# Optimization experiments

Hardware: AMD Instinct MI355X
Metric: run time of the kernel (lower is better)

Reference implementation:

```python
import jax, jax.numpy as jnp
import numpy as np

ENT_TOTAL = 500000
REL_TOTAL = 1000
H = 128
B = 1024
K = 10  # negative_ent + negative_rel
MARGIN = 1.0


def setup_inputs() -> dict:
    key = jax.random.key(0)
    ks = jax.random.split(key, 8)
    return {
        "ent_embeddings": jax.random.normal(ks[0], (ENT_TOTAL, H), dtype=jnp.float32) * 0.05,
        "rel_matrices": jax.random.normal(ks[1], (REL_TOTAL, H * H), dtype=jnp.float32) * 0.05,
        "pos_h": jax.random.randint(ks[2], (B,), 0, ENT_TOTAL, dtype=jnp.int32),
        "pos_t": jax.random.randint(ks[3], (B,), 0, ENT_TOTAL, dtype=jnp.int32),
        "pos_r": jax.random.randint(ks[4], (B,), 0, REL_TOTAL, dtype=jnp.int32),
        "neg_h": jax.random.randint(ks[5], (B * K,), 0, ENT_TOTAL, dtype=jnp.int32),
        "neg_t": jax.random.randint(ks[6], (B * K,), 0, ENT_TOTAL, dtype=jnp.int32),
        "neg_r": jax.random.randint(ks[7], (B * K,), 0, REL_TOTAL, dtype=jnp.int32),
    }


def _calc_score(ent_emb, rel_mat, h_idx, t_idx, r_idx):
    # gather embeddings / relation matrices per example
    h = ent_emb[h_idx]                          # [N, H]
    t = ent_emb[t_idx]                          # [N, H]
    r = rel_mat[r_idx].reshape(-1, H, H)        # [N, H, H]
    # h * (r @ t), then sum over hidden dim -> per-example score [N]
    rt = jnp.einsum('nij,nj->ni', r, t)         # [N, H]
    return jnp.sum(h * rt, axis=-1)             # [N]


def reference(ent_embeddings, rel_matrices, pos_h, pos_t, pos_r, neg_h, neg_t, neg_r):
    p_score = _calc_score(ent_embeddings, rel_matrices, pos_h, pos_t, pos_r)  # [B]
    n_all = _calc_score(ent_embeddings, rel_matrices, neg_h, neg_t, neg_r)    # [B*K]
    # mean over the K negatives per positive (matches reduce_mean over axis 1)
    n_score = jnp.mean(n_all.reshape(B, K), axis=1)                           # [B]
    loss = jnp.sum(jnp.maximum(n_score - p_score + MARGIN, 0.0))
    return loss
```

## Files before the change

kernel.cpp:

```cpp
#include <hip/hip_runtime.h>

#define H 128
#define BPOS 1024
#define KNEG 10
#define NPOS 1024
#define NNEG (BPOS * KNEG)
#define NTOT (NPOS + NNEG)

__global__ __launch_bounds__(256) void rescal_score_kernel(
    const float* __restrict__ ent,
    const float* __restrict__ rel,
    const int* __restrict__ pos_h, const int* __restrict__ pos_t,
    const int* __restrict__ pos_r,
    const int* __restrict__ neg_h, const int* __restrict__ neg_t,
    const int* __restrict__ neg_r,
    float* __restrict__ scores)
{
    const int n   = blockIdx.x;
    const int tid = threadIdx.x;

    int h_idx, t_idx, r_idx;
    if (n < NPOS) {
        h_idx = pos_h[n]; t_idx = pos_t[n]; r_idx = pos_r[n];
    } else {
        const int m = n - NPOS;
        h_idx = neg_h[m]; t_idx = neg_t[m]; r_idx = neg_r[m];
    }

    __shared__ float sh[H];
    __shared__ float st[H];
    if (tid < H) {
        sh[tid] = ent[(size_t)h_idx * H + tid];
    } else {
        st[tid - H] = ent[(size_t)t_idx * H + (tid - H)];
    }
    __syncthreads();

    const float4* __restrict__ R4 =
        (const float4*)(rel + (size_t)r_idx * (H * H));

    const int jbase = (4 * tid) & 127;
    const float4 t4 = *(const float4*)&st[jbase];

    float acc = 0.0f;
    const int ibase = tid >> 5;
#pragma unroll
    for (int k = 0; k < 16; ++k) {
        const float4 r4 = R4[k * 256 + tid];
        const float  hi = sh[8 * k + ibase];
        acc += hi * (r4.x * t4.x + r4.y * t4.y + r4.z * t4.z + r4.w * t4.w);
    }

#pragma unroll
    for (int off = 32; off > 0; off >>= 1)
        acc += __shfl_down(acc, off, 64);

    __shared__ float red[4];
    const int wave = tid >> 6;
    if ((tid & 63) == 0) red[wave] = acc;
    __syncthreads();
    if (tid == 0)
        scores[n] = red[0] + red[1] + red[2] + red[3];
}

__global__ __launch_bounds__(1024) void rescal_loss_kernel(
    const float* __restrict__ scores,
    float* __restrict__ out)
{
    const int b = threadIdx.x;
    const float p = scores[b];
    const float* __restrict__ neg = scores + NPOS + b * KNEG;
    float ns = 0.0f;
#pragma unroll
    for (int k = 0; k < KNEG; ++k) ns += neg[k];
    ns *= (1.0f / KNEG);

    float l = fmaxf(ns - p + 1.0f, 0.0f);

#pragma unroll
    for (int off = 32; off > 0; off >>= 1)
        l += __shfl_down(l, off, 64);

    __shared__ float red[16];
    const int wave = b >> 6;
    if ((b & 63) == 0) red[wave] = l;
    __syncthreads();
    if (b == 0) {
        float s = 0.0f;
#pragma unroll
        for (int w = 0; w < 16; ++w) s += red[w];
        out[0] = s;
    }
}

extern "C" void kernel_launch(void* const* d_in, const int* in_sizes, int n_in,
                              void* d_out, int out_size, void* d_ws, size_t ws_size,
                              hipStream_t stream) {
    const float* ent   = (const float*)d_in[0];
    const float* rel   = (const float*)d_in[1];
    const int* pos_h   = (const int*)d_in[2];
    const int* pos_t   = (const int*)d_in[3];
    const int* pos_r   = (const int*)d_in[4];
    const int* neg_h   = (const int*)d_in[5];
    const int* neg_t   = (const int*)d_in[6];
    const int* neg_r   = (const int*)d_in[7];

    float* scores = (float*)d_ws;
    float* out    = (float*)d_out;

    rescal_score_kernel<<<NTOT, 256, 0, stream>>>(
        ent, rel, pos_h, pos_t, pos_r, neg_h, neg_t, neg_r, scores);
    rescal_loss_kernel<<<1, 1024, 0, stream>>>(scores, out);
}
```

Measured before the change: 407.3 us.

## Group examples by relation so each relation matrix is loaded once

The kernel now launches one block per relation instead of one block per example. Each block stages its 128x128 relation matrix in shared memory, scans every example's relation index to build a list of matching examples, then computes their scores one wave at a time, prefetching the next example's head and tail embeddings. This removes the repeated global reads of a 64KB matrix per example. In exchange, every block scans all relation indices, and the per-relation list is capped at 256 entries, so any relation used by more examples would silently drop scores.

```diff
diff --git a/kernel.cpp b/kernel.cpp
--- a/kernel.cpp
+++ b/kernel.cpp
@@ -1,13 +1,14 @@
 #include <hip/hip_runtime.h>
 
 #define H 128
-#define BPOS 1024
+#define NPOS 1024
 #define KNEG 10
-#define NPOS 1024
-#define NNEG (BPOS * KNEG)
+#define NNEG (NPOS * KNEG)
 #define NTOT (NPOS + NNEG)
+#define NREL 1000
+#define MAXL 256
 
-__global__ __launch_bounds__(256) void rescal_score_kernel(
+__global__ __launch_bounds__(256) void rescal_rel_kernel(
     const float* __restrict__ ent,
     const float* __restrict__ rel,
     const int* __restrict__ pos_h, const int* __restrict__ pos_t,
@@ -16,51 +17,92 @@
     const int* __restrict__ neg_r,
     float* __restrict__ scores)
 {
-    const int n   = blockIdx.x;
+    const int r   = blockIdx.x;
     const int tid = threadIdx.x;
 
-    int h_idx, t_idx, r_idx;
-    if (n < NPOS) {
-        h_idx = pos_h[n]; t_idx = pos_t[n]; r_idx = pos_r[n];
-    } else {
-        const int m = n - NPOS;
-        h_idx = neg_h[m]; t_idx = neg_t[m]; r_idx = neg_r[m];
+    __shared__ float sR[H * H];
+    __shared__ float sht[4][2][H];
+    __shared__ int   list[MAXL];
+    __shared__ int   cnt;
+
+    if (tid == 0) cnt = 0;
+    __syncthreads();
+
+    {
+        const float4* __restrict__ Rg = (const float4*)(rel + (size_t)r * (H * H));
+        float4* __restrict__ Rs = (float4*)sR;
+#pragma unroll
+        for (int m = 0; m < 16; ++m)
+            Rs[m * 256 + tid] = Rg[m * 256 + tid];
     }
 
-    __shared__ float sh[H];
-    __shared__ float st[H];
-    if (tid < H) {
-        sh[tid] = ent[(size_t)h_idx * H + tid];
-    } else {
-        st[tid - H] = ent[(size_t)t_idx * H + (tid - H)];
+    for (int n = tid; n < NTOT; n += 256) {
+        const int rn = (n < NPOS) ? pos_r[n] : neg_r[n - NPOS];
+        if (rn == r) {
+            const int p = atomicAdd(&cnt, 1);
+            if (p < MAXL) list[p] = n;
+        }
     }
     __syncthreads();
 
-    const float4* __restrict__ R4 =
-        (const float4*)(rel + (size_t)r_idx * (H * H));
+    const int m    = cnt < MAXL ? cnt : MAXL;
+    const int wave = tid >> 6;
+    const int lane = tid & 63;
+    const int half = lane >> 5;
+    const int jcb  = lane & 31;
 
-    const int jbase = (4 * tid) & 127;
-    const float4 t4 = *(const float4*)&st[jbase];
+    float* __restrict__ hslot = sht[wave][0];
+    float* __restrict__ tslot = sht[wave][1];
 
-    float acc = 0.0f;
-    const int ibase = tid >> 5;
-#pragma unroll
-    for (int k = 0; k < 16; ++k) {
-        const float4 r4 = R4[k * 256 + tid];
-        const float  hi = sh[8 * k + ibase];
-        acc += hi * (r4.x * t4.x + r4.y * t4.y + r4.z * t4.z + r4.w * t4.w);
+    int idx = wave;
+    float2 ph = make_float2(0.f, 0.f), pt = make_float2(0.f, 0.f);
+    if (idx < m) {
+        const int n  = list[idx];
+        const int hi = (n < NPOS) ? pos_h[n] : neg_h[n - NPOS];
+        const int ti = (n < NPOS) ? pos_t[n] : neg_t[n - NPOS];
+        ph = ((const float2*)(ent + (size_t)hi * H))[lane];
+        pt = ((const float2*)(ent + (size_t)ti * H))[lane];
     }
 
+    while (idx < m) {
+        const int n = list[idx];
+
+        ((float2*)hslot)[lane] = ph;
+        ((float2*)tslot)[lane] = pt;
+        asm volatile("s_waitcnt lgkmcnt(0)" ::: "memory");
+
+        const int nidx = idx + 4;
+        if (nidx < m) {
+            const int n2 = list[nidx];
+            const int hi = (n2 < NPOS) ? pos_h[n2] : neg_h[n2 - NPOS];
+            const int ti = (n2 < NPOS) ? pos_t[n2] : neg_t[n2 - NPOS];
+            ph = ((const float2*)(ent + (size_t)hi * H))[lane];
+            pt = ((const float2*)(ent + (size_t)ti * H))[lane];
+        }
+
+        const float4  t4  = *(const float4*)&tslot[4 * jcb];
+        const float4* hs4 = (const float4*)&hslot[half * 64];
+        const float4* Rr4 = (const float4*)&sR[(size_t)half * 64 * H];
+
+        float acc = 0.f;
 #pragma unroll
-    for (int off = 32; off > 0; off >>= 1)
-        acc += __shfl_down(acc, off, 64);
+        for (int kk = 0; kk < 16; ++kk) {
+            const float4 h4 = hs4[kk];
+#pragma unroll
+            for (int d = 0; d < 4; ++d) {
+                const float4 r4 = Rr4[(kk * 4 + d) * 32 + jcb];
+                const float  hv = (d == 0) ? h4.x : (d == 1) ? h4.y : (d == 2) ? h4.z : h4.w;
+                acc += hv * (r4.x * t4.x + r4.y * t4.y + r4.z * t4.z + r4.w * t4.w);
+            }
+        }
 
-    __shared__ float red[4];
-    const int wave = tid >> 6;
-    if ((tid & 63) == 0) red[wave] = acc;
-    __syncthreads();
-    if (tid == 0)
-        scores[n] = red[0] + red[1] + red[2] + red[3];
+#pragma unroll
+        for (int mask = 32; mask > 0; mask >>= 1)
+            acc += __shfl_xor(acc, mask, 64);
+        if (lane == 0) scores[n] = acc;
+
+        idx = nidx;
+    }
 }
 
 __global__ __launch_bounds__(1024) void rescal_loss_kernel(
@@ -108,7 +150,7 @@
     float* scores = (float*)d_ws;
     float* out    = (float*)d_out;
 
-    rescal_score_kernel<<<NTOT, 256, 0, stream>>>(
+    rescal_rel_kernel<<<NREL, 256, 0, stream>>>(
         ent, rel, pos_h, pos_t, pos_r, neg_h, neg_t, neg_r, scores);
     rescal_loss_kernel<<<1, 1024, 0, stream>>>(scores, out);
 }
```

After: 371.9 us. 1.1x faster.
